# Optimization experiments

Measured on AMD Instinct MI355X. Metric: run time of the kernel, lower is better.

The kernel has to match this reference:

```python
import jax, jax.numpy as jnp
import numpy as np
import math

D_MODEL = 1024
N_HEAD = 16
Q_DIM = K_DIM = V_DIM = 1024
SCALE = math.sqrt(D_MODEL // N_HEAD)  # 8.0
B, LQ, LK = 2, 2048, 2048


def setup_inputs() -> dict:
    key = jax.random.key(0)
    ks = jax.random.split(key, 10)
    s = 1.0 / math.sqrt(Q_DIM)
    return {
        "q": jax.random.normal(ks[0], (B, LQ, Q_DIM), jnp.float32),
        "k": jax.random.normal(ks[1], (B, LK, K_DIM), jnp.float32),
        "v": jax.random.normal(ks[2], (B, LK, V_DIM), jnp.float32),
        "mask": jax.random.randint(ks[3], (B, LQ, LK), 0, 2, jnp.int32),
        "Wq": jax.random.uniform(ks[4], (D_MODEL, Q_DIM), jnp.float32, -s, s),
        "bq": jnp.zeros((D_MODEL,), jnp.float32),
        "Wk": jax.random.uniform(ks[5], (D_MODEL, K_DIM), jnp.float32, -s, s),
        "bk": jnp.zeros((D_MODEL,), jnp.float32),
        "Wv": jax.random.uniform(ks[6], (D_MODEL, V_DIM), jnp.float32, -s, s),
        "bv": jnp.zeros((D_MODEL,), jnp.float32),
    }


def reference(q, k, v, Wq, bq, Wk, bk, Wv, bv, mask):
    b, lq, _ = q.shape
    lk = k.shape[1]
    dh = D_MODEL // N_HEAD
    # linear projections (torch Linear: x @ W.T + b)
    qh = (q @ Wq.T + bq).reshape(b, lq, N_HEAD, dh).transpose(0, 2, 1, 3)  # bhqd
    kh = (k @ Wk.T + bk).reshape(b, lk, N_HEAD, dh).transpose(0, 2, 1, 3)  # bhkd
    vh = (v @ Wv.T + bv).reshape(b, lk, N_HEAD, dh).transpose(0, 2, 1, 3)  # bhkd
    attn = jnp.einsum("bhqd,bhkd->bhqk", qh, kh) / SCALE
    m = mask[:, None, :, :]  # b1qk
    attn = jnp.where(m == 0, -jnp.inf, attn)
    # rows whose mask is all-zero are reset to 0 pre-softmax (-> uniform weights)
    row_empty = (m.sum(-1, keepdims=True) == 0)
    attn = jnp.where(row_empty, 0.0, attn)
    attn = jax.nn.softmax(attn, axis=-1)  # dropout is identity in eval mode
    v_out = jnp.einsum("bhqk,bhkd->bhqd", attn, vh)
    v_out = v_out.transpose(0, 2, 1, 3).reshape(b, lq, D_MODEL)
    k_out = jnp.einsum("bhqk,bhkd->bhqd", attn, kh)
    k_out = k_out.transpose(0, 2, 1, 3).reshape(b, lq, D_MODEL)
    return (k_out, v_out)
```

## Files before the change

### kernel.cpp

```cpp
#include <hip/hip_runtime.h>
#include <hip/hip_bf16.h>
#include <stdint.h>

typedef __bf16 bf16x8 __attribute__((ext_vector_type(8)));
typedef __bf16 bf16x4 __attribute__((ext_vector_type(4)));
typedef float f32x4 __attribute__((ext_vector_type(4)));

#define B_ 2
#define LQ_ 2048
#define LK_ 2048
#define NH_ 16
#define DH_ 64
#define DM_ 1024
#define NKT_ (LK_ / 64)

#define AS1 __attribute__((address_space(1)))
#define AS3 __attribute__((address_space(3)))

__device__ __forceinline__ void gload_lds16(const void* g, void* l) {
  __builtin_amdgcn_global_load_lds((const AS1 uint32_t*)g, (AS3 uint32_t*)l, 16, 0, 0);
}

__global__ __launch_bounds__(256) void pack_mask_kernel(
    const int* __restrict__ m, unsigned* __restrict__ out) {
  int gtid = blockIdx.x * 256 + threadIdx.x;
  unsigned long long bal = __ballot(m[gtid] != 0);
  if ((threadIdx.x & 31) == 0)
    out[gtid >> 5] = (unsigned)(bal >> ((threadIdx.x & 32) ? 32 : 0));
}

__global__ __launch_bounds__(256) void cvt6_kernel(
    const float* __restrict__ q, const float* __restrict__ k,
    const float* __restrict__ v, const float* __restrict__ wq,
    const float* __restrict__ wk, const float* __restrict__ wv,
    __bf16* __restrict__ X0, __bf16* __restrict__ X1, __bf16* __restrict__ X2,
    __bf16* __restrict__ W0, __bf16* __restrict__ W1, __bf16* __restrict__ W2) {
  int seg = blockIdx.y;
  if (seg >= 3 && blockIdx.x >= DM_ * DM_ / 1024) return;
  const float* s = seg == 0 ? q : seg == 1 ? k : seg == 2 ? v
                  : seg == 3 ? wq : seg == 4 ? wk : wv;
  __bf16* d = seg == 0 ? X0 : seg == 1 ? X1 : seg == 2 ? X2
             : seg == 3 ? W0 : seg == 4 ? W1 : W2;
  size_t t = (size_t)blockIdx.x * 256 + threadIdx.x;
  float4 f = ((const float4*)s)[t];
  bf16x4 o;
  o[0] = (__bf16)f.x; o[1] = (__bf16)f.y; o[2] = (__bf16)f.z; o[3] = (__bf16)f.w;
  ((bf16x4*)d)[t] = o;
}

__global__ __launch_bounds__(256) void proj_kernel(
    const __bf16* __restrict__ X0, const __bf16* __restrict__ X1,
    const __bf16* __restrict__ X2,
    const float* __restrict__ b0p, const float* __restrict__ b1p,
    const float* __restrict__ b2p,
    const __bf16* __restrict__ W0, const __bf16* __restrict__ W1,
    const __bf16* __restrict__ W2,
    __bf16* __restrict__ qh, __bf16* __restrict__ kh,
    __bf16* __restrict__ khT, __bf16* __restrict__ vhT) {
  __shared__ __align__(16) __bf16 smem[128 * 72];
  __bf16* abuf = smem;
  __bf16* bbuf = smem + 128 * 32;
  __bf16* cbuf = smem;

  const int mode = blockIdx.z;
  const __bf16* X = mode == 0 ? X0 : (mode == 1 ? X1 : X2);
  const __bf16* W = mode == 0 ? W0 : (mode == 1 ? W1 : W2);
  const float* bias = mode == 0 ? b0p : (mode == 1 ? b1p : b2p);
  __bf16* ostd = mode == 0 ? qh : (mode == 1 ? kh : nullptr);
  __bf16* otr = mode == 0 ? nullptr : (mode == 1 ? khT : vhT);

  const int t = threadIdx.x;
  const int wave = t >> 6, lane = t & 63;
  const int lo16 = lane & 15, quad = lane >> 4;
  const int wm = wave >> 1, wn = wave & 1;
  const int m0 = blockIdx.x * 128, n0 = blockIdx.y * 128;
  const int srow = lane >> 2, scg = (lane & 3) ^ (srow & 3);

  f32x4 acc[4][4] = {};

  for (int k0 = 0; k0 < DM_; k0 += 32) {
    __syncthreads();
#pragma unroll
    for (int ii = 2 * wave; ii < 2 * wave + 2; ii++) {
      int row = ii * 16 + srow;
      gload_lds16(X + (size_t)(m0 + row) * DM_ + k0 + scg * 8, abuf + ii * 512);
      gload_lds16(W + (size_t)(n0 + row) * DM_ + k0 + scg * 8, bbuf + ii * 512);
    }
    __syncthreads();
    bf16x8 af[4], bfr[4];
#pragma unroll
    for (int g = 0; g < 4; g++) {
      int ar = wm * 64 + g * 16 + lo16;
      af[g] = *(const bf16x8*)(abuf + ar * 32 + (quad ^ (ar & 3)) * 8);
      int br = wn * 64 + g * 16 + lo16;
      bfr[g] = *(const bf16x8*)(bbuf + br * 32 + (quad ^ (br & 3)) * 8);
    }
#pragma unroll
    for (int gm = 0; gm < 4; gm++)
#pragma unroll
      for (int gn = 0; gn < 4; gn++)
        acc[gm][gn] =
            __builtin_amdgcn_mfma_f32_16x16x32_bf16(af[gm], bfr[gn], acc[gm][gn], 0, 0, 0);
  }

  const int b = m0 >> 11, l0 = m0 & 2047;
  for (int nhf = 0; nhf < 2; nhf++) {
    int h = (n0 >> 6) + nhf;
    int bh = b * NH_ + h;
    if (ostd) {
      __syncthreads();
      if (wn == nhf) {
#pragma unroll
        for (int gn = 0; gn < 4; gn++) {
          float bi = bias[n0 + nhf * 64 + gn * 16 + lo16];
#pragma unroll
          for (int gm = 0; gm < 4; gm++)
#pragma unroll
            for (int r = 0; r < 4; r++)
              cbuf[(wm * 64 + gm * 16 + quad * 4 + r) * 72 + gn * 16 + lo16] =
                  (__bf16)(acc[gm][gn][r] + bi);
        }
      }
      __syncthreads();
      int m = t >> 1, coff = (t & 1) * 32;
      __bf16* dst = ostd + ((size_t)bh * LQ_ + l0 + m) * DH_ + coff;
#pragma unroll
      for (int j = 0; j < 4; j++)
        *(bf16x8*)(dst + j * 8) = *(const bf16x8*)&cbuf[m * 72 + coff + j * 8];
    }
    if (otr) {
      __syncthreads();
      if (wn == nhf) {
#pragma unroll
        for (int gn = 0; gn < 4; gn++) {
          float bi = bias[n0 + nhf * 64 + gn * 16 + lo16];
#pragma unroll
          for (int gm = 0; gm < 4; gm++) {
            bf16x4 pk;
#pragma unroll
            for (int r = 0; r < 4; r++) pk[r] = (__bf16)(acc[gm][gn][r] + bi);
            *(bf16x4*)&cbuf[(gn * 16 + lo16) * 136 + wm * 64 + gm * 16 + quad * 4] = pk;
          }
        }
      }
      __syncthreads();
      int d = t >> 2, mc = (t & 3) * 32;
      int kti = (l0 + mc) >> 6, kl = (l0 + mc) & 63;
      __bf16* dst = otr + ((size_t)(bh * NKT_ + kti) * 64 + d) * 64 + kl;
#pragma unroll
      for (int j = 0; j < 4; j++)
        *(bf16x8*)(dst + j * 8) = *(const bf16x8*)&cbuf[d * 136 + mc + j * 8];
    }
  }
}

__global__ __launch_bounds__(256) void attn_kernel(
    const __bf16* __restrict__ qh, const __bf16* __restrict__ kh,
    const __bf16* __restrict__ khT, const __bf16* __restrict__ vhT,
    const unsigned* __restrict__ maskp,
    float* __restrict__ out_k, float* __restrict__ out_v) {
  __shared__ __align__(16) __bf16 kbuf[2][64 * 64];
  __shared__ __align__(16) __bf16 ktbuf[2][64 * 64];
  __shared__ __align__(16) __bf16 vtbuf[2][64 * 64];
  __shared__ __align__(16) __bf16 p_lds[4][2][16][72];

  const int t = threadIdx.x;
  const int wave = t >> 6, lane = t & 63;
  const int lo16 = lane & 15, quad = lane >> 4;
  const int bh = blockIdx.x;
  const int b = bh >> 4, h = bh & 15;
  const int q0 = blockIdx.y * 128 + wave * 16;
  const int srow = lane >> 3;
  const int scg = (lane & 7) ^ srow;
  const int rsw = lo16 & 7;

  bf16x8 a_q0[2], a_q1[2];
#pragma unroll
  for (int g = 0; g < 2; g++) {
    const __bf16* qrow = qh + ((size_t)bh * LQ_ + q0 + g * 64 + lo16) * DH_ + quad * 8;
    a_q0[g] = *(const bf16x8*)(qrow);
    a_q1[g] = *(const bf16x8*)(qrow + 32);
  }

  f32x4 acc_v[2][4] = {};
  f32x4 acc_k[2][4] = {};
  float lsum[2][4] = {};

  const __bf16* khb = kh + (size_t)bh * LK_ * DH_;
  const __bf16* ktb = khT + (size_t)bh * LK_ * DH_;
  const __bf16* vtb = vhT + (size_t)bh * LK_ * DH_;

  auto stage = [&](int kti, int sel) {
    const int tb = kti * 4096;
#pragma unroll
    for (int ii = 2 * wave; ii < 2 * wave + 2; ii++) {
      int row = ii * 8 + srow;
      gload_lds16(khb + (size_t)(kti * 64 + row) * DH_ + scg * 8, &kbuf[sel][ii * 512]);
      gload_lds16(ktb + tb + row * 64 + scg * 8, &ktbuf[sel][ii * 512]);
      gload_lds16(vtb + tb + row * 64 + scg * 8, &vtbuf[sel][ii * 512]);
    }
  };

  stage(0, 0);
  for (int kti = 0; kti < NKT_; kti++) {
    const int cur = kti & 1, nxt = cur ^ 1;
    __syncthreads();
    if (kti + 1 < NKT_) stage(kti + 1, nxt);
#pragma unroll
    for (int g = 0; g < 2; g++) {
      f32x4 s[4];
#pragma unroll
      for (int gg = 0; gg < 4; gg++) {
        int row = gg * 16 + lo16;
        bf16x8 kb0 = *(const bf16x8*)(&kbuf[cur][row * 64 + ((quad ^ rsw) * 8)]);
        bf16x8 kb1 = *(const bf16x8*)(&kbuf[cur][row * 64 + (((quad + 4) ^ rsw) * 8)]);
        f32x4 z = {};
        z = __builtin_amdgcn_mfma_f32_16x16x32_bf16(a_q0[g], kb0, z, 0, 0, 0);
        z = __builtin_amdgcn_mfma_f32_16x16x32_bf16(a_q1[g], kb1, z, 0, 0, 0);
        s[gg] = z;
      }
      const unsigned* mb =
          maskp + ((size_t)b * LQ_ + q0 + g * 64 + quad * 4) * (LK_ / 32);
      unsigned mw0[4], mw1[4];
#pragma unroll
      for (int r = 0; r < 4; r++) {
        mw0[r] = mb[r * (LK_ / 32) + kti * 2];
        mw1[r] = mb[r * (LK_ / 32) + kti * 2 + 1];
      }
#pragma unroll
      for (int gg = 0; gg < 4; gg++) {
        int bitpos = (gg * 16 + lo16) & 31;
#pragma unroll
        for (int r = 0; r < 4; r++) {
          unsigned w = (gg >= 2) ? mw1[r] : mw0[r];
          float arg = ((w >> bitpos) & 1) ? s[gg][r] * 0.125f : -28.0f;
          float p = __expf(arg);
          s[gg][r] = p;
          lsum[g][r] += p;
        }
      }
#pragma unroll
      for (int gg = 0; gg < 4; gg++) {
#pragma unroll
        for (int r = 0; r < 4; r++)
          p_lds[wave][g][quad * 4 + r][gg * 16 + lo16] = (__bf16)s[gg][r];
      }
      bf16x8 a_p0 = *(const bf16x8*)&p_lds[wave][g][lo16][quad * 8];
      bf16x8 a_p1 = *(const bf16x8*)&p_lds[wave][g][lo16][32 + quad * 8];
#pragma unroll
      for (int gg = 0; gg < 4; gg++) {
        int row = gg * 16 + lo16;
        bf16x8 bv0 = *(const bf16x8*)(&vtbuf[cur][row * 64 + ((quad ^ rsw) * 8)]);
        bf16x8 bv1 = *(const bf16x8*)(&vtbuf[cur][row * 64 + (((quad + 4) ^ rsw) * 8)]);
        acc_v[g][gg] = __builtin_amdgcn_mfma_f32_16x16x32_bf16(a_p0, bv0, acc_v[g][gg], 0, 0, 0);
        acc_v[g][gg] = __builtin_amdgcn_mfma_f32_16x16x32_bf16(a_p1, bv1, acc_v[g][gg], 0, 0, 0);
        bf16x8 bk0 = *(const bf16x8*)(&ktbuf[cur][row * 64 + ((quad ^ rsw) * 8)]);
        bf16x8 bk1 = *(const bf16x8*)(&ktbuf[cur][row * 64 + (((quad + 4) ^ rsw) * 8)]);
        acc_k[g][gg] = __builtin_amdgcn_mfma_f32_16x16x32_bf16(a_p0, bk0, acc_k[g][gg], 0, 0, 0);
        acc_k[g][gg] = __builtin_amdgcn_mfma_f32_16x16x32_bf16(a_p1, bk1, acc_k[g][gg], 0, 0, 0);
      }
    }
  }

#pragma unroll
  for (int off = 1; off < 16; off <<= 1) {
#pragma unroll
    for (int g = 0; g < 2; g++)
#pragma unroll
      for (int r = 0; r < 4; r++) lsum[g][r] += __shfl_xor(lsum[g][r], off, 64);
  }
#pragma unroll
  for (int g = 0; g < 2; g++) {
    float inv_l[4];
#pragma unroll
    for (int r = 0; r < 4; r++) inv_l[r] = 1.0f / lsum[g][r];
    size_t obase = ((size_t)b * LQ_ + q0 + g * 64 + quad * 4) * DM_ + h * DH_;
#pragma unroll
    for (int gg = 0; gg < 4; gg++) {
#pragma unroll
      for (int r = 0; r < 4; r++) {
        size_t idx = obase + (size_t)r * DM_ + gg * 16 + lo16;
        out_k[idx] = acc_k[g][gg][r] * inv_l[r];
        out_v[idx] = acc_v[g][gg][r] * inv_l[r];
      }
    }
  }
}

extern "C" void kernel_launch(void* const* d_in, const int* in_sizes, int n_in,
                              void* d_out, int out_size, void* d_ws, size_t ws_size,
                              hipStream_t stream) {
  const float* q = (const float*)d_in[0];
  const float* k = (const float*)d_in[1];
  const float* v = (const float*)d_in[2];
  const int* mask = (const int*)d_in[3];
  const float* Wq = (const float*)d_in[4];
  const float* bq = (const float*)d_in[5];
  const float* Wk = (const float*)d_in[6];
  const float* bk = (const float*)d_in[7];
  const float* Wv = (const float*)d_in[8];
  const float* bv = (const float*)d_in[9];
  float* out = (float*)d_out;

  const size_t HTOT = (size_t)B_ * NH_ * LQ_ * DH_;
  const size_t XTOT = (size_t)B_ * LQ_ * DM_;
  __bf16* qh = (__bf16*)d_ws;
  __bf16* kh = qh + HTOT;
  __bf16* khT = kh + HTOT;
  __bf16* vhT = khT + HTOT;
  unsigned* maskp = (unsigned*)(vhT + HTOT);

  __bf16* X0 = (__bf16*)d_out;
  __bf16* X1 = X0 + XTOT;
  __bf16* X2 = X1 + XTOT;
  __bf16* W0 = X2 + XTOT;
  __bf16* W1 = W0 + (size_t)DM_ * DM_;
  __bf16* W2 = W1 + (size_t)DM_ * DM_;

  pack_mask_kernel<<<(B_ * LQ_ * LK_) / 256, 256, 0, stream>>>(mask, maskp);
  cvt6_kernel<<<dim3(XTOT / 1024, 6), 256, 0, stream>>>(
      q, k, v, Wq, Wk, Wv, X0, X1, X2, W0, W1, W2);
  proj_kernel<<<dim3(32, 8, 3), 256, 0, stream>>>(
      X0, X1, X2, bq, bk, bv, W0, W1, W2, qh, kh, khT, vhT);
  attn_kernel<<<dim3(32, 16), 256, 0, stream>>>(qh, kh, khT, vhT, maskp,
                                                out, out + (size_t)B_ * LQ_ * DM_);
}
```

Measured before the change: 291.8 us.

## Double-buffer projection GEMM and shrink attention tile with shuffle-based P transpose

The projection GEMM now double-buffers its LDS tiles so the global-to-LDS load of the next K slice overlaps the MFMAs on the current one. The attention kernel processes 64 query rows per block instead of 128, doubling the grid, and sets launch bounds to three blocks per CU. It computes S transposed (K as the A operand) so that P can be re-laid out with cross-lane shuffles instead of a round trip through LDS. This cuts LDS traffic and registers and raises occupancy, but K/V tiles are now loaded twice as often per query row.

```diff
diff --git a/kernel.cpp b/kernel.cpp
--- a/kernel.cpp
+++ b/kernel.cpp
@@ -57,10 +57,8 @@
     const __bf16* __restrict__ W2,
     __bf16* __restrict__ qh, __bf16* __restrict__ kh,
     __bf16* __restrict__ khT, __bf16* __restrict__ vhT) {
-  __shared__ __align__(16) __bf16 smem[128 * 72];
-  __bf16* abuf = smem;
-  __bf16* bbuf = smem + 128 * 32;
-  __bf16* cbuf = smem;
+  __shared__ __align__(16) __bf16 smem[2][2][128 * 32];
+  __bf16* cbuf = &smem[0][0][0];
 
   const int mode = blockIdx.z;
   const __bf16* X = mode == 0 ? X0 : (mode == 1 ? X1 : X2);
@@ -78,22 +76,27 @@
 
   f32x4 acc[4][4] = {};
 
-  for (int k0 = 0; k0 < DM_; k0 += 32) {
-    __syncthreads();
+  auto stage = [&](int k0, int sel) {
 #pragma unroll
     for (int ii = 2 * wave; ii < 2 * wave + 2; ii++) {
       int row = ii * 16 + srow;
-      gload_lds16(X + (size_t)(m0 + row) * DM_ + k0 + scg * 8, abuf + ii * 512);
-      gload_lds16(W + (size_t)(n0 + row) * DM_ + k0 + scg * 8, bbuf + ii * 512);
-    }
+      gload_lds16(X + (size_t)(m0 + row) * DM_ + k0 + scg * 8, &smem[sel][0][ii * 512]);
+      gload_lds16(W + (size_t)(n0 + row) * DM_ + k0 + scg * 8, &smem[sel][1][ii * 512]);
+    }
+  };
+
+  stage(0, 0);
+  for (int k0 = 0; k0 < DM_; k0 += 32) {
+    const int sel = (k0 >> 5) & 1;
     __syncthreads();
+    if (k0 + 32 < DM_) stage(k0 + 32, sel ^ 1);
     bf16x8 af[4], bfr[4];
 #pragma unroll
     for (int g = 0; g < 4; g++) {
       int ar = wm * 64 + g * 16 + lo16;
-      af[g] = *(const bf16x8*)(abuf + ar * 32 + (quad ^ (ar & 3)) * 8);
+      af[g] = *(const bf16x8*)(&smem[sel][0][ar * 32 + (quad ^ (ar & 3)) * 8]);
       int br = wn * 64 + g * 16 + lo16;
-      bfr[g] = *(const bf16x8*)(bbuf + br * 32 + (quad ^ (br & 3)) * 8);
+      bfr[g] = *(const bf16x8*)(&smem[sel][1][br * 32 + (quad ^ (br & 3)) * 8]);
     }
 #pragma unroll
     for (int gm = 0; gm < 4; gm++)
@@ -154,7 +157,7 @@
   }
 }
 
-__global__ __launch_bounds__(256) void attn_kernel(
+__global__ __launch_bounds__(256, 3) void attn_kernel(
     const __bf16* __restrict__ qh, const __bf16* __restrict__ kh,
     const __bf16* __restrict__ khT, const __bf16* __restrict__ vhT,
     const unsigned* __restrict__ maskp,
@@ -162,33 +165,29 @@
   __shared__ __align__(16) __bf16 kbuf[2][64 * 64];
   __shared__ __align__(16) __bf16 ktbuf[2][64 * 64];
   __shared__ __align__(16) __bf16 vtbuf[2][64 * 64];
-  __shared__ __align__(16) __bf16 p_lds[4][2][16][72];
 
   const int t = threadIdx.x;
   const int wave = t >> 6, lane = t & 63;
   const int lo16 = lane & 15, quad = lane >> 4;
   const int bh = blockIdx.x;
   const int b = bh >> 4, h = bh & 15;
-  const int q0 = blockIdx.y * 128 + wave * 16;
+  const int q0 = blockIdx.y * 64 + wave * 16;
   const int srow = lane >> 3;
   const int scg = (lane & 7) ^ srow;
   const int rsw = lo16 & 7;
 
-  bf16x8 a_q0[2], a_q1[2];
-#pragma unroll
-  for (int g = 0; g < 2; g++) {
-    const __bf16* qrow = qh + ((size_t)bh * LQ_ + q0 + g * 64 + lo16) * DH_ + quad * 8;
-    a_q0[g] = *(const bf16x8*)(qrow);
-    a_q1[g] = *(const bf16x8*)(qrow + 32);
-  }
-
-  f32x4 acc_v[2][4] = {};
-  f32x4 acc_k[2][4] = {};
-  float lsum[2][4] = {};
+  const __bf16* qrow = qh + ((size_t)bh * LQ_ + q0 + lo16) * DH_ + quad * 8;
+  bf16x8 a_q0 = *(const bf16x8*)(qrow);
+  bf16x8 a_q1 = *(const bf16x8*)(qrow + 32);
+
+  f32x4 acc_v[4] = {};
+  f32x4 acc_k[4] = {};
+  float lsum = 0.f;
 
   const __bf16* khb = kh + (size_t)bh * LK_ * DH_;
   const __bf16* ktb = khT + (size_t)bh * LK_ * DH_;
   const __bf16* vtb = vhT + (size_t)bh * LK_ * DH_;
+  const unsigned* mb = maskp + ((size_t)b * LQ_ + q0 + lo16) * (LK_ / 32);
 
   auto stage = [&](int kti, int sel) {
     const int tb = kti * 4096;
@@ -203,86 +202,90 @@
 
   stage(0, 0);
   for (int kti = 0; kti < NKT_; kti++) {
-    const int cur = kti & 1, nxt = cur ^ 1;
+    const int cur = kti & 1;
     __syncthreads();
-    if (kti + 1 < NKT_) stage(kti + 1, nxt);
-#pragma unroll
-    for (int g = 0; g < 2; g++) {
-      f32x4 s[4];
-#pragma unroll
-      for (int gg = 0; gg < 4; gg++) {
-        int row = gg * 16 + lo16;
-        bf16x8 kb0 = *(const bf16x8*)(&kbuf[cur][row * 64 + ((quad ^ rsw) * 8)]);
-        bf16x8 kb1 = *(const bf16x8*)(&kbuf[cur][row * 64 + (((quad + 4) ^ rsw) * 8)]);
-        f32x4 z = {};
-        z = __builtin_amdgcn_mfma_f32_16x16x32_bf16(a_q0[g], kb0, z, 0, 0, 0);
-        z = __builtin_amdgcn_mfma_f32_16x16x32_bf16(a_q1[g], kb1, z, 0, 0, 0);
-        s[gg] = z;
+    if (kti + 1 < NKT_) stage(kti + 1, cur ^ 1);
+
+    f32x4 s[4];
+#pragma unroll
+    for (int gg = 0; gg < 4; gg++) {
+      int row = gg * 16 + lo16;
+      bf16x8 ka0 = *(const bf16x8*)(&kbuf[cur][row * 64 + ((quad ^ rsw) * 8)]);
+      bf16x8 ka1 = *(const bf16x8*)(&kbuf[cur][row * 64 + (((quad + 4) ^ rsw) * 8)]);
+      f32x4 z = {};
+      z = __builtin_amdgcn_mfma_f32_16x16x32_bf16(ka0, a_q0, z, 0, 0, 0);
+      z = __builtin_amdgcn_mfma_f32_16x16x32_bf16(ka1, a_q1, z, 0, 0, 0);
+      s[gg] = z;
+    }
+    unsigned mw0 = mb[kti * 2], mw1 = mb[kti * 2 + 1];
+#pragma unroll
+    for (int gg = 0; gg < 4; gg++) {
+      unsigned w = (gg < 2) ? mw0 : mw1;
+      int bitbase = (gg & 1) * 16 + quad * 4;
+#pragma unroll
+      for (int r = 0; r < 4; r++) {
+        float arg = ((w >> (bitbase + r)) & 1) ? s[gg][r] * 0.125f : -28.0f;
+        float p = __expf(arg);
+        s[gg][r] = p;
+        lsum += p;
       }
-      const unsigned* mb =
-          maskp + ((size_t)b * LQ_ + q0 + g * 64 + quad * 4) * (LK_ / 32);
-      unsigned mw0[4], mw1[4];
-#pragma unroll
-      for (int r = 0; r < 4; r++) {
-        mw0[r] = mb[r * (LK_ / 32) + kti * 2];
-        mw1[r] = mb[r * (LK_ / 32) + kti * 2 + 1];
-      }
-#pragma unroll
-      for (int gg = 0; gg < 4; gg++) {
-        int bitpos = (gg * 16 + lo16) & 31;
-#pragma unroll
-        for (int r = 0; r < 4; r++) {
-          unsigned w = (gg >= 2) ? mw1[r] : mw0[r];
-          float arg = ((w >> bitpos) & 1) ? s[gg][r] * 0.125f : -28.0f;
-          float p = __expf(arg);
-          s[gg][r] = p;
-          lsum[g][r] += p;
-        }
-      }
-#pragma unroll
-      for (int gg = 0; gg < 4; gg++) {
-#pragma unroll
-        for (int r = 0; r < 4; r++)
-          p_lds[wave][g][quad * 4 + r][gg * 16 + lo16] = (__bf16)s[gg][r];
-      }
-      bf16x8 a_p0 = *(const bf16x8*)&p_lds[wave][g][lo16][quad * 8];
-      bf16x8 a_p1 = *(const bf16x8*)&p_lds[wave][g][lo16][32 + quad * 8];
-#pragma unroll
-      for (int gg = 0; gg < 4; gg++) {
-        int row = gg * 16 + lo16;
-        bf16x8 bv0 = *(const bf16x8*)(&vtbuf[cur][row * 64 + ((quad ^ rsw) * 8)]);
-        bf16x8 bv1 = *(const bf16x8*)(&vtbuf[cur][row * 64 + (((quad + 4) ^ rsw) * 8)]);
-        acc_v[g][gg] = __builtin_amdgcn_mfma_f32_16x16x32_bf16(a_p0, bv0, acc_v[g][gg], 0, 0, 0);
-        acc_v[g][gg] = __builtin_amdgcn_mfma_f32_16x16x32_bf16(a_p1, bv1, acc_v[g][gg], 0, 0, 0);
-        bf16x8 bk0 = *(const bf16x8*)(&ktbuf[cur][row * 64 + ((quad ^ rsw) * 8)]);
-        bf16x8 bk1 = *(const bf16x8*)(&ktbuf[cur][row * 64 + (((quad + 4) ^ rsw) * 8)]);
-        acc_k[g][gg] = __builtin_amdgcn_mfma_f32_16x16x32_bf16(a_p0, bk0, acc_k[g][gg], 0, 0, 0);
-        acc_k[g][gg] = __builtin_amdgcn_mfma_f32_16x16x32_bf16(a_p1, bk1, acc_k[g][gg], 0, 0, 0);
-      }
+    }
+    int pkl[4], pkh[4];
+#pragma unroll
+    for (int gg = 0; gg < 4; gg++) {
+      union { bf16x4 h; int2 i; } u;
+      u.h[0] = (__bf16)s[gg][0]; u.h[1] = (__bf16)s[gg][1];
+      u.h[2] = (__bf16)s[gg][2]; u.h[3] = (__bf16)s[gg][3];
+      pkl[gg] = u.i.x; pkh[gg] = u.i.y;
+    }
+    const int S0 = (quad & 1) * 32 + lo16;
+    const int S1 = S0 + 16;
+    const bool hiq = quad >= 2;
+    union { int4 i; bf16x8 h; } w0, w1;
+    {
+      int x0 = __shfl(pkl[0], S0, 64), x1 = __shfl(pkh[0], S0, 64);
+      int x2 = __shfl(pkl[0], S1, 64), x3 = __shfl(pkh[0], S1, 64);
+      int y0 = __shfl(pkl[1], S0, 64), y1 = __shfl(pkh[1], S0, 64);
+      int y2 = __shfl(pkl[1], S1, 64), y3 = __shfl(pkh[1], S1, 64);
+      w0.i = make_int4(hiq ? y0 : x0, hiq ? y1 : x1, hiq ? y2 : x2, hiq ? y3 : x3);
+    }
+    {
+      int x0 = __shfl(pkl[2], S0, 64), x1 = __shfl(pkh[2], S0, 64);
+      int x2 = __shfl(pkl[2], S1, 64), x3 = __shfl(pkh[2], S1, 64);
+      int y0 = __shfl(pkl[3], S0, 64), y1 = __shfl(pkh[3], S0, 64);
+      int y2 = __shfl(pkl[3], S1, 64), y3 = __shfl(pkh[3], S1, 64);
+      w1.i = make_int4(hiq ? y0 : x0, hiq ? y1 : x1, hiq ? y2 : x2, hiq ? y3 : x3);
+    }
+    bf16x8 a_p0 = w0.h;
+    bf16x8 a_p1 = w1.h;
+#pragma unroll
+    for (int gg = 0; gg < 4; gg++) {
+      int row = gg * 16 + lo16;
+      bf16x8 bv0 = *(const bf16x8*)(&vtbuf[cur][row * 64 + ((quad ^ rsw) * 8)]);
+      bf16x8 bv1 = *(const bf16x8*)(&vtbuf[cur][row * 64 + (((quad + 4) ^ rsw) * 8)]);
+      acc_v[gg] = __builtin_amdgcn_mfma_f32_16x16x32_bf16(a_p0, bv0, acc_v[gg], 0, 0, 0);
+      acc_v[gg] = __builtin_amdgcn_mfma_f32_16x16x32_bf16(a_p1, bv1, acc_v[gg], 0, 0, 0);
+      bf16x8 bk0 = *(const bf16x8*)(&ktbuf[cur][row * 64 + ((quad ^ rsw) * 8)]);
+      bf16x8 bk1 = *(const bf16x8*)(&ktbuf[cur][row * 64 + (((quad + 4) ^ rsw) * 8)]);
+      acc_k[gg] = __builtin_amdgcn_mfma_f32_16x16x32_bf16(a_p0, bk0, acc_k[gg], 0, 0, 0);
+      acc_k[gg] = __builtin_amdgcn_mfma_f32_16x16x32_bf16(a_p1, bk1, acc_k[gg], 0, 0, 0);
     }
   }
 
-#pragma unroll
-  for (int off = 1; off < 16; off <<= 1) {
-#pragma unroll
-    for (int g = 0; g < 2; g++)
-#pragma unroll
-      for (int r = 0; r < 4; r++) lsum[g][r] += __shfl_xor(lsum[g][r], off, 64);
-  }
-#pragma unroll
-  for (int g = 0; g < 2; g++) {
-    float inv_l[4];
-#pragma unroll
-    for (int r = 0; r < 4; r++) inv_l[r] = 1.0f / lsum[g][r];
-    size_t obase = ((size_t)b * LQ_ + q0 + g * 64 + quad * 4) * DM_ + h * DH_;
-#pragma unroll
-    for (int gg = 0; gg < 4; gg++) {
-#pragma unroll
-      for (int r = 0; r < 4; r++) {
-        size_t idx = obase + (size_t)r * DM_ + gg * 16 + lo16;
-        out_k[idx] = acc_k[g][gg][r] * inv_l[r];
-        out_v[idx] = acc_v[g][gg][r] * inv_l[r];
-      }
+  lsum += __shfl_xor(lsum, 16, 64);
+  lsum += __shfl_xor(lsum, 32, 64);
+  float inv_l[4];
+#pragma unroll
+  for (int r = 0; r < 4; r++) inv_l[r] = 1.0f / __shfl(lsum, quad * 4 + r, 64);
+
+  size_t obase = ((size_t)b * LQ_ + q0 + quad * 4) * DM_ + h * DH_;
+#pragma unroll
+  for (int gg = 0; gg < 4; gg++) {
+#pragma unroll
+    for (int r = 0; r < 4; r++) {
+      size_t idx = obase + (size_t)r * DM_ + gg * 16 + lo16;
+      out_k[idx] = acc_k[gg][r] * inv_l[r];
+      out_v[idx] = acc_v[gg][r] * inv_l[r];
     }
   }
 }
@@ -322,6 +325,6 @@
       q, k, v, Wq, Wk, Wv, X0, X1, X2, W0, W1, W2);
   proj_kernel<<<dim3(32, 8, 3), 256, 0, stream>>>(
       X0, X1, X2, bq, bk, bv, W0, W1, W2, qh, kh, khT, vhT);
-  attn_kernel<<<dim3(32, 16), 256, 0, stream>>>(qh, kh, khT, vhT, maskp,
+  attn_kernel<<<dim3(32, 32), 256, 0, stream>>>(qh, kh, khT, vhT, maskp,
                                                 out, out + (size_t)B_ * LQ_ * DM_);
 }
```

Result: no change. 293.2 us (+0.5%).

## Fuse mask pack and conversion into one prep kernel with k-tiled layout

Applied to the files above, without the earlier changes.

Merges the mask-packing and fp32-to-bf16 conversion kernels into one launch. The conversion now writes the projection operands in a k-tile-major, pre-swizzled layout, so each projection stage is a single contiguous 512-byte load per row group. The projection GEMM gains double-buffered LDS with prefetch of the next k-tile, which removes one barrier per iteration. The intent is to cut a launch and overlap global loads with MFMA work, at the cost of a staging pass through LDS in the prep kernel and twice the LDS footprint in the projection.

```diff
diff --git a/kernel.cpp b/kernel.cpp
--- a/kernel.cpp
+++ b/kernel.cpp
@@ -21,50 +21,71 @@
   __builtin_amdgcn_global_load_lds((const AS1 uint32_t*)g, (AS3 uint32_t*)l, 16, 0, 0);
 }
 
-__global__ __launch_bounds__(256) void pack_mask_kernel(
-    const int* __restrict__ m, unsigned* __restrict__ out) {
-  int gtid = blockIdx.x * 256 + threadIdx.x;
-  unsigned long long bal = __ballot(m[gtid] != 0);
-  if ((threadIdx.x & 31) == 0)
-    out[gtid >> 5] = (unsigned)(bal >> ((threadIdx.x & 32) ? 32 : 0));
-}
-
-__global__ __launch_bounds__(256) void cvt6_kernel(
+__global__ __launch_bounds__(256) void prep_kernel(
     const float* __restrict__ q, const float* __restrict__ k,
     const float* __restrict__ v, const float* __restrict__ wq,
     const float* __restrict__ wk, const float* __restrict__ wv,
-    __bf16* __restrict__ X0, __bf16* __restrict__ X1, __bf16* __restrict__ X2,
-    __bf16* __restrict__ W0, __bf16* __restrict__ W1, __bf16* __restrict__ W2) {
-  int seg = blockIdx.y;
-  if (seg >= 3 && blockIdx.x >= DM_ * DM_ / 1024) return;
-  const float* s = seg == 0 ? q : seg == 1 ? k : seg == 2 ? v
-                  : seg == 3 ? wq : seg == 4 ? wk : wv;
-  __bf16* d = seg == 0 ? X0 : seg == 1 ? X1 : seg == 2 ? X2
-             : seg == 3 ? W0 : seg == 4 ? W1 : W2;
-  size_t t = (size_t)blockIdx.x * 256 + threadIdx.x;
-  float4 f = ((const float4*)s)[t];
-  bf16x4 o;
-  o[0] = (__bf16)f.x; o[1] = (__bf16)f.y; o[2] = (__bf16)f.z; o[3] = (__bf16)f.w;
-  ((bf16x4*)d)[t] = o;
+    const int* __restrict__ mask,
+    __bf16* __restrict__ Xt0, __bf16* __restrict__ Xt1, __bf16* __restrict__ Xt2,
+    __bf16* __restrict__ Wt0, __bf16* __restrict__ Wt1, __bf16* __restrict__ Wt2,
+    unsigned* __restrict__ maskp) {
+  const int t = threadIdx.x;
+  const int bidx = blockIdx.x;
+  if (bidx >= 960) {
+    int pb = bidx - 960;
+    int lane = t & 63;
+    size_t gi = ((size_t)pb * 256 + t) * 4;
+    int4 mv = *(const int4*)(mask + gi);
+    unsigned nib = (mv.x != 0 ? 1u : 0u) | (mv.y != 0 ? 2u : 0u) |
+                   (mv.z != 0 ? 4u : 0u) | (mv.w != 0 ? 8u : 0u);
+    unsigned vv = nib << ((lane & 7) * 4);
+    vv |= __shfl_xor(vv, 1, 64);
+    vv |= __shfl_xor(vv, 2, 64);
+    vv |= __shfl_xor(vv, 4, 64);
+    if ((lane & 7) == 0) maskp[gi >> 5] = vv;
+    return;
+  }
+  __shared__ __align__(16) __bf16 lb[16][1032];
+  const float* src; __bf16* dst; int rows, m0;
+  if (bidx < 256)      { src = q;  dst = Xt0; rows = 4096; m0 = bidx * 16; }
+  else if (bidx < 512) { src = k;  dst = Xt1; rows = 4096; m0 = (bidx - 256) * 16; }
+  else if (bidx < 768) { src = v;  dst = Xt2; rows = 4096; m0 = (bidx - 512) * 16; }
+  else if (bidx < 832) { src = wq; dst = Wt0; rows = 1024; m0 = (bidx - 768) * 16; }
+  else if (bidx < 896) { src = wk; dst = Wt1; rows = 1024; m0 = (bidx - 832) * 16; }
+  else                 { src = wv; dst = Wt2; rows = 1024; m0 = (bidx - 896) * 16; }
+#pragma unroll
+  for (int i = 0; i < 16; i++) {
+    float4 f = *(const float4*)(src + (size_t)(m0 + i) * DM_ + t * 4);
+    bf16x4 o;
+    o[0] = (__bf16)f.x; o[1] = (__bf16)f.y; o[2] = (__bf16)f.z; o[3] = (__bf16)f.w;
+    *(bf16x4*)&lb[i][t * 4] = o;
+  }
+  __syncthreads();
+  const int wave = t >> 6, lane = t & 63;
+  const int m = lane >> 2, c = lane & 3;
+#pragma unroll
+  for (int j = 0; j < 8; j++) {
+    int kt = wave * 8 + j;
+    bf16x8 val = *(const bf16x8*)&lb[m][kt * 32 + (c ^ (m & 3)) * 8];
+    *(bf16x8*)(dst + ((size_t)kt * rows + m0 + m) * 32 + c * 8) = val;
+  }
 }
 
 __global__ __launch_bounds__(256) void proj_kernel(
-    const __bf16* __restrict__ X0, const __bf16* __restrict__ X1,
-    const __bf16* __restrict__ X2,
+    const __bf16* __restrict__ Xt0, const __bf16* __restrict__ Xt1,
+    const __bf16* __restrict__ Xt2,
     const float* __restrict__ b0p, const float* __restrict__ b1p,
     const float* __restrict__ b2p,
-    const __bf16* __restrict__ W0, const __bf16* __restrict__ W1,
-    const __bf16* __restrict__ W2,
+    const __bf16* __restrict__ Wt0, const __bf16* __restrict__ Wt1,
+    const __bf16* __restrict__ Wt2,
     __bf16* __restrict__ qh, __bf16* __restrict__ kh,
     __bf16* __restrict__ khT, __bf16* __restrict__ vhT) {
-  __shared__ __align__(16) __bf16 smem[128 * 72];
-  __bf16* abuf = smem;
-  __bf16* bbuf = smem + 128 * 32;
-  __bf16* cbuf = smem;
+  __shared__ __align__(16) __bf16 smem[2][2][128 * 32];
+  __bf16* cbuf = &smem[0][0][0];
 
   const int mode = blockIdx.z;
-  const __bf16* X = mode == 0 ? X0 : (mode == 1 ? X1 : X2);
-  const __bf16* W = mode == 0 ? W0 : (mode == 1 ? W1 : W2);
+  const __bf16* Xt = mode == 0 ? Xt0 : (mode == 1 ? Xt1 : Xt2);
+  const __bf16* Wt = mode == 0 ? Wt0 : (mode == 1 ? Wt1 : Wt2);
   const float* bias = mode == 0 ? b0p : (mode == 1 ? b1p : b2p);
   __bf16* ostd = mode == 0 ? qh : (mode == 1 ? kh : nullptr);
   __bf16* otr = mode == 0 ? nullptr : (mode == 1 ? khT : vhT);
@@ -74,26 +95,31 @@
   const int lo16 = lane & 15, quad = lane >> 4;
   const int wm = wave >> 1, wn = wave & 1;
   const int m0 = blockIdx.x * 128, n0 = blockIdx.y * 128;
-  const int srow = lane >> 2, scg = (lane & 3) ^ (srow & 3);
 
   f32x4 acc[4][4] = {};
 
-  for (int k0 = 0; k0 < DM_; k0 += 32) {
+  auto stage = [&](int kt, int sel) {
+#pragma unroll
+    for (int ii = 2 * wave; ii < 2 * wave + 2; ii++) {
+      gload_lds16(Xt + ((size_t)kt * 4096 + m0 + ii * 16) * 32 + lane * 8,
+                  &smem[sel][0][ii * 512]);
+      gload_lds16(Wt + ((size_t)kt * 1024 + n0 + ii * 16) * 32 + lane * 8,
+                  &smem[sel][1][ii * 512]);
+    }
+  };
+
+  stage(0, 0);
+  for (int kt = 0; kt < 32; kt++) {
+    const int sel = kt & 1;
     __syncthreads();
-#pragma unroll
-    for (int ii = 2 * wave; ii < 2 * wave + 2; ii++) {
-      int row = ii * 16 + srow;
-      gload_lds16(X + (size_t)(m0 + row) * DM_ + k0 + scg * 8, abuf + ii * 512);
-      gload_lds16(W + (size_t)(n0 + row) * DM_ + k0 + scg * 8, bbuf + ii * 512);
-    }
-    __syncthreads();
+    if (kt + 1 < 32) stage(kt + 1, sel ^ 1);
     bf16x8 af[4], bfr[4];
 #pragma unroll
     for (int g = 0; g < 4; g++) {
       int ar = wm * 64 + g * 16 + lo16;
-      af[g] = *(const bf16x8*)(abuf + ar * 32 + (quad ^ (ar & 3)) * 8);
+      af[g] = *(const bf16x8*)(&smem[sel][0][ar * 32 + (quad ^ (ar & 3)) * 8]);
       int br = wn * 64 + g * 16 + lo16;
-      bfr[g] = *(const bf16x8*)(bbuf + br * 32 + (quad ^ (br & 3)) * 8);
+      bfr[g] = *(const bf16x8*)(&smem[sel][1][br * 32 + (quad ^ (br & 3)) * 8]);
     }
 #pragma unroll
     for (int gm = 0; gm < 4; gm++)
@@ -203,9 +229,9 @@
 
   stage(0, 0);
   for (int kti = 0; kti < NKT_; kti++) {
-    const int cur = kti & 1, nxt = cur ^ 1;
+    const int cur = kti & 1;
     __syncthreads();
-    if (kti + 1 < NKT_) stage(kti + 1, nxt);
+    if (kti + 1 < NKT_) stage(kti + 1, cur ^ 1);
 #pragma unroll
     for (int g = 0; g < 2; g++) {
       f32x4 s[4];
@@ -310,18 +336,17 @@
   __bf16* vhT = khT + HTOT;
   unsigned* maskp = (unsigned*)(vhT + HTOT);
 
-  __bf16* X0 = (__bf16*)d_out;
-  __bf16* X1 = X0 + XTOT;
-  __bf16* X2 = X1 + XTOT;
-  __bf16* W0 = X2 + XTOT;
-  __bf16* W1 = W0 + (size_t)DM_ * DM_;
-  __bf16* W2 = W1 + (size_t)DM_ * DM_;
-
-  pack_mask_kernel<<<(B_ * LQ_ * LK_) / 256, 256, 0, stream>>>(mask, maskp);
-  cvt6_kernel<<<dim3(XTOT / 1024, 6), 256, 0, stream>>>(
-      q, k, v, Wq, Wk, Wv, X0, X1, X2, W0, W1, W2);
+  __bf16* Xt0 = (__bf16*)d_out;
+  __bf16* Xt1 = Xt0 + XTOT;
+  __bf16* Xt2 = Xt1 + XTOT;
+  __bf16* Wt0 = Xt2 + XTOT;
+  __bf16* Wt1 = Wt0 + (size_t)DM_ * DM_;
+  __bf16* Wt2 = Wt1 + (size_t)DM_ * DM_;
+
+  prep_kernel<<<960 + 8192, 256, 0, stream>>>(
+      q, k, v, Wq, Wk, Wv, mask, Xt0, Xt1, Xt2, Wt0, Wt1, Wt2, maskp);
   proj_kernel<<<dim3(32, 8, 3), 256, 0, stream>>>(
-      X0, X1, X2, bq, bk, bv, W0, W1, W2, qh, kh, khT, vhT);
+      Xt0, Xt1, Xt2, bq, bk, bv, Wt0, Wt1, Wt2, qh, kh, khT, vhT);
   attn_kernel<<<dim3(32, 16), 256, 0, stream>>>(qh, kh, khT, vhT, maskp,
                                                 out, out + (size_t)B_ * LQ_ * DM_);
 }
```

Result: faster. 280.4 us (-3.9%).
